# Kernel tuning notes

Measured on AMD Instinct MI355X. Metric: run time of the kernel, lower is better.

## Reference

```python
import jax, jax.numpy as jnp
import numpy as np

B, N, D, H = 4, 4096, 1024, 16
HD = D // H  # 64
EPS_NORM = 1e-12  # F.normalize eps
EPS_LN = 1e-5     # layernorm eps


def setup_inputs() -> dict:
    key = jax.random.key(0)
    ks = jax.random.split(key, 9)
    s = 0.02
    return {
        "x": jax.random.normal(ks[0], (B, N, D), jnp.float32),
        "Wq": jax.random.normal(ks[1], (D, D), jnp.float32) * s,
        "Wk": jax.random.normal(ks[2], (D, D), jnp.float32) * s,
        "Wv": jax.random.normal(ks[3], (D, D), jnp.float32) * s,
        "Wf": jax.random.normal(ks[4], (H, D), jnp.float32) * s,
        "Wg1": jax.random.normal(ks[5], (HD, D), jnp.float32) * s,
        "Wg2": jax.random.normal(ks[6], (D, HD), jnp.float32) * s,
        "ln_w": jnp.ones((D,), jnp.float32),
        "Wo": jax.random.normal(ks[7], (D, D), jnp.float32) * s,
    }


def _silu(x):
    return x * jax.nn.sigmoid(x)


def _simple_gla(q, k, v, f):
    # q,k,v: [B,N,H,HD], f: [B,N,H] log-decay. Recurrence:
    #   S_t = exp(f_t) * S_{t-1} + k_t v_t^T ;  o_t = q_t^T S_t  (scale=1)
    qT = jnp.moveaxis(q, 1, 0)  # [N,B,H,HD]
    kT = jnp.moveaxis(k, 1, 0)
    vT = jnp.moveaxis(v, 1, 0)
    fT = jnp.moveaxis(f, 1, 0)  # [N,B,H]

    def step(S, inp):
        qt, kt, vt, ft = inp
        S = jnp.exp(ft)[..., None, None] * S + kt[..., :, None] * vt[..., None, :]
        o = jnp.einsum('bhk,bhkv->bhv', qt, S)
        return S, o

    S0 = jnp.zeros((q.shape[0], q.shape[2], q.shape[3], v.shape[3]), q.dtype)
    _, o = jax.lax.scan(step, S0, (qT, kT, vT, fT))
    return jnp.moveaxis(o, 0, 1)  # [B,N,H,HD]


def reference(x, Wq, Wk, Wv, Wf, Wg1, Wg2, ln_w, Wo):
    b, n, d = x.shape
    q = _silu(x @ Wq.T).reshape(b, n, H, HD)
    k = _silu(x @ Wk.T).reshape(b, n, H, HD)
    v = _silu(x @ Wv.T).reshape(b, n, H, HD)
    f = jax.nn.log_sigmoid(x @ Wf.T)  # [B,N,H] scalar per-head log decay
    # F.normalize(k, p=2, dim=-1)
    k = k / jnp.maximum(jnp.linalg.norm(k, axis=-1, keepdims=True), EPS_NORM)

    o = _simple_gla(q, k, v, f).reshape(b, n, d)

    # output gate: sigmoid(Linear(d->hd) -> Linear(hd->d))
    gate = jax.nn.sigmoid((x @ Wg1.T) @ Wg2.T)
    o = o * gate

    # layernorm without bias
    mu = jnp.mean(o, axis=-1, keepdims=True)
    xc = o - mu
    var = jnp.mean(xc * xc, axis=-1, keepdims=True)
    o = xc / jnp.sqrt(var + EPS_LN) * ln_w

    return o @ Wo.T
```

## Files before the change

kernel.cpp:

```cpp
#include <hip/hip_runtime.h>
#include <stdint.h>


#define NWIDE 3200

typedef __attribute__((ext_vector_type(4))) float f32x4;
typedef __attribute__((ext_vector_type(4))) unsigned short u16x4;
typedef __attribute__((ext_vector_type(8))) unsigned short u16x8;
typedef __attribute__((ext_vector_type(8))) __bf16 bf16x8;

__device__ __forceinline__ float bf2f(unsigned short u) {
    union { unsigned int i; float f; } c; c.i = ((unsigned int)u) << 16; return c.f;
}
__device__ __forceinline__ unsigned short f2bf(float f) {
    union { float f; unsigned int i; } c; c.f = f;
    return (unsigned short)((c.i + 0x7fffu + ((c.i >> 16) & 1u)) >> 16);
}
__device__ __forceinline__ float siluf(float x) { return x / (1.f + __expf(-x)); }
__device__ __forceinline__ float logsigf(float z) {
    return (z >= 0.f) ? -log1pf(__expf(-z)) : (z - log1pf(__expf(z)));
}
__device__ __forceinline__ f32x4 MFMA(bf16x8 a, bf16x8 b, f32x4 c) {
    return __builtin_amdgcn_mfma_f32_16x16x32_bf16(a, b, c, 0, 0, 0);
}
__device__ __forceinline__ void lds16(const void* g, void* l) {
    __builtin_amdgcn_global_load_lds(
        (const __attribute__((address_space(1))) unsigned int*)(uintptr_t)g,
        (__attribute__((address_space(3))) unsigned int*)(unsigned int)(uintptr_t)l,
        16, 0, 0);
}

__global__ __launch_bounds__(256) void k_convert(const float* __restrict__ src,
                                                 unsigned short* __restrict__ dst, int n4) {
    int i = blockIdx.x * 256 + threadIdx.x;
    if (i >= n4) return;
    f32x4 v = ((const f32x4*)src)[i];
    u16x4 o;
#pragma unroll
    for (int e = 0; e < 4; e++) o[e] = f2bf(v[e]);
    ((u16x4*)dst)[i] = o;
}

__global__ __launch_bounds__(256) void k_wcat(const float* __restrict__ Wq, const float* __restrict__ Wk,
                                              const float* __restrict__ Wv, const float* __restrict__ Wf,
                                              const float* __restrict__ Wg1, unsigned short* __restrict__ Wcat) {
    const int r = blockIdx.x, t = threadIdx.x;
    const float* src = nullptr; int sr = r;
    if (r < 1024) { src = Wq; }
    else if (r < 2048) { src = Wk; sr = r - 1024; }
    else if (r < 3072) { src = Wv; sr = r - 2048; }
    else if (r < 3088) { src = Wf; sr = r - 3072; }
    else if (r < 3152) { src = Wg1; sr = r - 3088; }
    u16x4 o;
    if (src) {
        f32x4 v = *(const f32x4*)&src[(size_t)sr * 1024 + 4 * t];
#pragma unroll
        for (int e = 0; e < 4; e++) o[e] = f2bf(v[e]);
    } else {
        o[0] = 0; o[1] = 0; o[2] = 0; o[3] = 0;
    }
    *(u16x4*)&Wcat[(size_t)r * 1024 + 4 * t] = o;
}

template <int MODE>
__global__ __launch_bounds__(256)
void k_gemm(const unsigned short* __restrict__ A, const unsigned short* __restrict__ Bw,
            void* __restrict__ outp, float* __restrict__ zbuf, int M, int N, int K, int ldOut) {
    __shared__ __align__(16) unsigned short As[128 * 32];
    __shared__ __align__(16) unsigned short Bs[128 * 32];
    const int tid = threadIdx.x;
    const int w = tid >> 6, lane = tid & 63;
    const int m0 = blockIdx.x * 128, n0 = blockIdx.y * 128;
    const int srow = lane >> 2, scol = (lane & 3) * 8;
    const int fr = lane & 15, fg = lane >> 4;
    const int wr = w >> 1, wc = w & 1;
    f32x4 acc[4][4] = {};
    const int kc = K >> 5;
    for (int kt = 0; kt < kc; ++kt) {
        const int k0 = kt << 5;
        __syncthreads();
        {
            const unsigned short* ga = A + (size_t)(m0 + 32 * w + srow) * K + k0 + scol;
            lds16(ga, &As[(32 * w) * 32]);
            const unsigned short* ga2 = A + (size_t)(m0 + 32 * w + 16 + srow) * K + k0 + scol;
            lds16(ga2, &As[(32 * w + 16) * 32]);
            const unsigned short* gb = Bw + (size_t)(n0 + 32 * w + srow) * K + k0 + scol;
            lds16(gb, &Bs[(32 * w) * 32]);
            const unsigned short* gb2 = Bw + (size_t)(n0 + 32 * w + 16 + srow) * K + k0 + scol;
            lds16(gb2, &Bs[(32 * w + 16) * 32]);
        }
        __syncthreads();
        bf16x8 av[4], bv[4];
#pragma unroll
        for (int i = 0; i < 4; i++) av[i] = *(const bf16x8*)&As[(64 * wr + 16 * i + fr) * 32 + fg * 8];
#pragma unroll
        for (int j = 0; j < 4; j++) bv[j] = *(const bf16x8*)&Bs[(64 * wc + 16 * j + fr) * 32 + fg * 8];
#pragma unroll
        for (int i = 0; i < 4; i++)
#pragma unroll
            for (int j = 0; j < 4; j++)
                acc[i][j] = MFMA(av[i], bv[j], acc[i][j]);
    }
    const int nb = n0 + 64 * wc;
    if (MODE == 1) {
        float* O = (float*)outp;
#pragma unroll
        for (int i = 0; i < 4; i++)
#pragma unroll
            for (int j = 0; j < 4; j++) {
                const int gc = nb + 16 * j + fr;
#pragma unroll
                for (int r = 0; r < 4; r++)
                    O[(size_t)(m0 + 64 * wr + 16 * i + 4 * fg + r) * ldOut + gc] = acc[i][j][r];
            }
        return;
    }
    unsigned short* Y = (unsigned short*)outp;
    if (nb >= 3072) {
#pragma unroll
        for (int i = 0; i < 4; i++)
#pragma unroll
            for (int j = 0; j < 4; j++) {
                const int gc = nb + 16 * j + fr;
#pragma unroll
                for (int r = 0; r < 4; r++) {
                    const int gr = m0 + 64 * wr + 16 * i + 4 * fg + r;
                    const float v = acc[i][j][r];
                    if (gc < 3088) {
                        if (gc >= 3072) zbuf[gr * 16 + (gc - 3072)] = v;
                    } else if (gc < 3152) {
                        Y[(size_t)gr * ldOut + gc] = f2bf(v);
                    }
                }
            }
    } else {
#pragma unroll
        for (int i = 0; i < 4; i++)
#pragma unroll
            for (int j = 0; j < 4; j++) {
                const int gc = nb + 16 * j + fr;
#pragma unroll
                for (int r = 0; r < 4; r++)
                    Y[(size_t)(m0 + 64 * wr + 16 * i + 4 * fg + r) * ldOut + gc] = f2bf(acc[i][j][r]);
            }
    }
}

__global__ void k_cumsum(const float* __restrict__ zbuf, float* __restrict__ cbuf) {
    const int cid = blockIdx.x, t = threadIdx.x;
    const int bh = cid >> 6, ic = cid & 63;
    const int b = bh >> 4, h = bh & 15;
    float v = logsigf(zbuf[(size_t)(b * 4096 + ic * 64 + t) * 16 + h]);
#pragma unroll
    for (int off = 1; off < 64; off <<= 1) {
        float u = __shfl_up(v, (unsigned)off, 64);
        if (t >= off) v += u;
    }
    cbuf[(size_t)cid * 64 + t] = v;
}

__global__ __launch_bounds__(256)
void k_chunk_kv(const unsigned short* __restrict__ Y, const float* __restrict__ cbuf,
                unsigned short* __restrict__ St) {
    __shared__ __align__(16) unsigned short Kt[64 * 72];
    __shared__ __align__(16) unsigned short Vt[64 * 72];
    __shared__ float cs[64];
    const int cid = blockIdx.x, tid = threadIdx.x;
    const int bh = cid >> 6, ic = cid & 63;
    const int b = bh >> 4, h = bh & 15;
    if (tid < 64) cs[tid] = cbuf[(size_t)cid * 64 + tid];
    __syncthreads();
    const int s = tid >> 2, c0 = (tid & 3) << 4;
    const float wdec = __expf(cs[63] - cs[s]);
    const size_t rowg = (size_t)(b * 4096 + ic * 64 + s) * NWIDE;
    u16x8 k0v = *(const u16x8*)&Y[rowg + 1024 + h * 64 + c0];
    u16x8 k1v = *(const u16x8*)&Y[rowg + 1024 + h * 64 + c0 + 8];
    u16x8 v0v = *(const u16x8*)&Y[rowg + 2048 + h * 64 + c0];
    u16x8 v1v = *(const u16x8*)&Y[rowg + 2048 + h * 64 + c0 + 8];
    float kf[16]; float ss = 0.f;
#pragma unroll
    for (int e = 0; e < 8; e++) { kf[e] = siluf(bf2f(k0v[e])); ss += kf[e] * kf[e]; }
#pragma unroll
    for (int e = 0; e < 8; e++) { kf[8 + e] = siluf(bf2f(k1v[e])); ss += kf[8 + e] * kf[8 + e]; }
    ss += __shfl_xor(ss, 1, 64);
    ss += __shfl_xor(ss, 2, 64);
    const float sc = wdec / fmaxf(sqrtf(ss), 1e-12f);
#pragma unroll
    for (int e = 0; e < 8; e++) {
        Kt[(c0 + e) * 72 + s] = f2bf(kf[e] * sc);
        Kt[(c0 + 8 + e) * 72 + s] = f2bf(kf[8 + e] * sc);
        Vt[(c0 + e) * 72 + s] = f2bf(siluf(bf2f(v0v[e])));
        Vt[(c0 + 8 + e) * 72 + s] = f2bf(siluf(bf2f(v1v[e])));
    }
    __syncthreads();
    const int w = tid >> 6, lane = tid & 63;
    const int fr = lane & 15, fg = lane >> 4;
    f32x4 acc[4] = {};
#pragma unroll
    for (int ks = 0; ks < 2; ks++) {
        bf16x8 a = *(const bf16x8*)&Kt[(16 * w + fr) * 72 + ks * 32 + fg * 8];
#pragma unroll
        for (int j = 0; j < 4; j++)
            acc[j] = MFMA(a, *(const bf16x8*)&Vt[(16 * j + fr) * 72 + ks * 32 + fg * 8], acc[j]);
    }
    unsigned short* outp = St + (size_t)cid * 4096;
#pragma unroll
    for (int j = 0; j < 4; j++)
#pragma unroll
        for (int r = 0; r < 4; r++)
            outp[(16 * w + 4 * fg + r) * 64 + 16 * j + fr] = f2bf(acc[j][r]);
}

__global__ void k_scan(unsigned short* __restrict__ St, const float* __restrict__ cbuf) {
    const int bh = blockIdx.x >> 4;
    const int e = ((blockIdx.x & 15) << 8) + threadIdx.x;
    float S = 0.f;
    const size_t base = (size_t)bh * 64 * 4096 + e;
    for (int i = 0; i < 64; i++) {
        const float d = __expf(cbuf[(bh * 64 + i) * 64 + 63]);
        const float m = bf2f(St[base + (size_t)i * 4096]);
        St[base + (size_t)i * 4096] = f2bf(S);
        S = d * S + m;
    }
}

__global__ __launch_bounds__(256)
void k_chunk_out(const unsigned short* __restrict__ Y, const float* __restrict__ cbuf,
                 const unsigned short* __restrict__ St, const unsigned short* __restrict__ Wg2b,
                 unsigned short* __restrict__ og) {
    __shared__ __align__(16) unsigned short Qs[64 * 72];
    __shared__ __align__(16) unsigned short Ks[64 * 72];
    __shared__ __align__(16) unsigned short Vt[64 * 72];
    __shared__ __align__(16) unsigned short S0[64 * 72];
    __shared__ __align__(16) unsigned short G1[64 * 72];
    __shared__ __align__(16) unsigned short W2[64 * 72];
    __shared__ __align__(16) unsigned short Pl[4 * 16 * 72];
    __shared__ float cs[64];
    const int cid = blockIdx.x, tid = threadIdx.x;
    const int bh = cid >> 6, ic = cid & 63;
    const int b = bh >> 4, h = bh & 15;
    if (tid < 64) cs[tid] = cbuf[(size_t)cid * 64 + tid];
    const int s = tid >> 2, c0 = (tid & 3) << 4;
    const size_t rowg = (size_t)(b * 4096 + ic * 64 + s) * NWIDE;
    {
        u16x8 q0 = *(const u16x8*)&Y[rowg + h * 64 + c0];
        u16x8 q1 = *(const u16x8*)&Y[rowg + h * 64 + c0 + 8];
        u16x8 o0, o1;
#pragma unroll
        for (int e = 0; e < 8; e++) { o0[e] = f2bf(siluf(bf2f(q0[e]))); o1[e] = f2bf(siluf(bf2f(q1[e]))); }
        *(u16x8*)&Qs[s * 72 + c0] = o0;
        *(u16x8*)&Qs[s * 72 + c0 + 8] = o1;
    }
    {
        u16x8 k0v = *(const u16x8*)&Y[rowg + 1024 + h * 64 + c0];
        u16x8 k1v = *(const u16x8*)&Y[rowg + 1024 + h * 64 + c0 + 8];
        float kf[16]; float ssn = 0.f;
#pragma unroll
        for (int e = 0; e < 8; e++) { kf[e] = siluf(bf2f(k0v[e])); ssn += kf[e] * kf[e]; }
#pragma unroll
        for (int e = 0; e < 8; e++) { kf[8 + e] = siluf(bf2f(k1v[e])); ssn += kf[8 + e] * kf[8 + e]; }
        ssn += __shfl_xor(ssn, 1, 64);
        ssn += __shfl_xor(ssn, 2, 64);
        const float scn = 1.f / fmaxf(sqrtf(ssn), 1e-12f);
        u16x8 o0, o1;
#pragma unroll
        for (int e = 0; e < 8; e++) { o0[e] = f2bf(kf[e] * scn); o1[e] = f2bf(kf[8 + e] * scn); }
        *(u16x8*)&Ks[s * 72 + c0] = o0;
        *(u16x8*)&Ks[s * 72 + c0 + 8] = o1;
    }
    *(u16x8*)&G1[s * 72 + c0] = *(const u16x8*)&Y[rowg + 3088 + c0];
    *(u16x8*)&G1[s * 72 + c0 + 8] = *(const u16x8*)&Y[rowg + 3088 + c0 + 8];
    *(u16x8*)&W2[s * 72 + c0] = *(const u16x8*)&Wg2b[(size_t)(h * 64 + s) * 64 + c0];
    *(u16x8*)&W2[s * 72 + c0 + 8] = *(const u16x8*)&Wg2b[(size_t)(h * 64 + s) * 64 + c0 + 8];
    {
        u16x8 v0v = *(const u16x8*)&Y[rowg + 2048 + h * 64 + c0];
        u16x8 v1v = *(const u16x8*)&Y[rowg + 2048 + h * 64 + c0 + 8];
        u16x8 s0v = *(const u16x8*)&St[(size_t)cid * 4096 + s * 64 + c0];
        u16x8 s1v = *(const u16x8*)&St[(size_t)cid * 4096 + s * 64 + c0 + 8];
#pragma unroll
        for (int e = 0; e < 8; e++) {
            Vt[(c0 + e) * 72 + s] = f2bf(siluf(bf2f(v0v[e])));
            Vt[(c0 + 8 + e) * 72 + s] = f2bf(siluf(bf2f(v1v[e])));
            S0[(c0 + e) * 72 + s] = s0v[e];
            S0[(c0 + 8 + e) * 72 + s] = s1v[e];
        }
    }
    __syncthreads();
    const int w = tid >> 6, lane = tid & 63;
    const int fr = lane & 15, fg = lane >> 4;
    bf16x8 aq[2];
#pragma unroll
    for (int ks = 0; ks < 2; ks++) aq[ks] = *(const bf16x8*)&Qs[(16 * w + fr) * 72 + ks * 32 + fg * 8];
    f32x4 sc[4] = {};
#pragma unroll
    for (int ks = 0; ks < 2; ks++)
#pragma unroll
        for (int j = 0; j < 4; j++)
            sc[j] = MFMA(aq[ks], *(const bf16x8*)&Ks[(16 * j + fr) * 72 + ks * 32 + fg * 8], sc[j]);
    const int tl = 16 * w + 4 * fg;
#pragma unroll
    for (int j = 0; j < 4; j++)
#pragma unroll
        for (int r = 0; r < 4; r++) {
            const int tt = tl + r, ss2 = 16 * j + fr;
            float p = (ss2 <= tt) ? sc[j][r] * __expf(cs[tt] - cs[ss2]) : 0.f;
            Pl[w * (16 * 72) + (4 * fg + r) * 72 + ss2] = f2bf(p);
        }
    __syncthreads();
    f32x4 ov[4] = {};
#pragma unroll
    for (int ks = 0; ks < 2; ks++) {
        bf16x8 ap = *(const bf16x8*)&Pl[w * (16 * 72) + fr * 72 + ks * 32 + fg * 8];
#pragma unroll
        for (int j = 0; j < 4; j++)
            ov[j] = MFMA(ap, *(const bf16x8*)&Vt[(16 * j + fr) * 72 + ks * 32 + fg * 8], ov[j]);
    }
    f32x4 qs[4] = {};
#pragma unroll
    for (int ks = 0; ks < 2; ks++)
#pragma unroll
        for (int j = 0; j < 4; j++)
            qs[j] = MFMA(aq[ks], *(const bf16x8*)&S0[(16 * j + fr) * 72 + ks * 32 + fg * 8], qs[j]);
    bf16x8 ag[2];
#pragma unroll
    for (int ks = 0; ks < 2; ks++) ag[ks] = *(const bf16x8*)&G1[(16 * w + fr) * 72 + ks * 32 + fg * 8];
    f32x4 gl[4] = {};
#pragma unroll
    for (int ks = 0; ks < 2; ks++)
#pragma unroll
        for (int j = 0; j < 4; j++)
            gl[j] = MFMA(ag[ks], *(const bf16x8*)&W2[(16 * j + fr) * 72 + ks * 32 + fg * 8], gl[j]);
#pragma unroll
    for (int j = 0; j < 4; j++)
#pragma unroll
        for (int r = 0; r < 4; r++) {
            const int tt = tl + r;
            const float o = ov[j][r] + __expf(cs[tt]) * qs[j][r];
            const float g = 1.f / (1.f + __expf(-gl[j][r]));
            og[(size_t)(b * 4096 + ic * 64 + tt) * 1024 + h * 64 + 16 * j + fr] = f2bf(o * g);
        }
}

__global__ __launch_bounds__(256)
void k_ln(unsigned short* __restrict__ og, const float* __restrict__ lnw) {
    __shared__ float red[8];
    const int r = blockIdx.x, t = threadIdx.x;
    unsigned short* p = og + (size_t)r * 1024;
    u16x4 a = *(u16x4*)&p[4 * t];
    float x[4]; float s = 0.f, ssum = 0.f;
#pragma unroll
    for (int e = 0; e < 4; e++) { x[e] = bf2f(a[e]); s += x[e]; ssum += x[e] * x[e]; }
#pragma unroll
    for (int m = 1; m < 64; m <<= 1) { s += __shfl_xor(s, m, 64); ssum += __shfl_xor(ssum, m, 64); }
    const int w = t >> 6;
    if ((t & 63) == 0) { red[w] = s; red[4 + w] = ssum; }
    __syncthreads();
    s = red[0] + red[1] + red[2] + red[3];
    ssum = red[4] + red[5] + red[6] + red[7];
    const float mu = s * (1.f / 1024.f);
    const float var = ssum * (1.f / 1024.f) - mu * mu;
    const float rs = rsqrtf(var + 1e-5f);
    u16x4 o;
#pragma unroll
    for (int e = 0; e < 4; e++) o[e] = f2bf((x[e] - mu) * rs * lnw[4 * t + e]);
    *(u16x4*)&p[4 * t] = o;
}

extern "C" void kernel_launch(void* const* d_in, const int* in_sizes, int n_in,
                              void* d_out, int out_size, void* d_ws, size_t ws_size,
                              hipStream_t stream) {
    const float* x = (const float*)d_in[0];
    const float* Wq = (const float*)d_in[1];
    const float* Wk = (const float*)d_in[2];
    const float* Wv = (const float*)d_in[3];
    const float* Wf = (const float*)d_in[4];
    const float* Wg1 = (const float*)d_in[5];
    const float* Wg2 = (const float*)d_in[6];
    const float* lnw = (const float*)d_in[7];
    const float* Wo = (const float*)d_in[8];
    char* ws = (char*)d_ws;
    unsigned short* xb = (unsigned short*)(ws + 0);
    unsigned short* Yb = (unsigned short*)(ws + 33554432LL);
    unsigned short* Wcat = (unsigned short*)(ws + 138412032LL);
    unsigned short* Wob = (unsigned short*)(ws + 144965632LL);
    unsigned short* Wg2b = (unsigned short*)(ws + 147062784LL);
    float* zbuf = (float*)(ws + 147193856LL);
    float* cbuf = (float*)(ws + 148242432LL);
    unsigned short* St = (unsigned short*)(ws + 149291008LL);
    unsigned short* og = xb;

    k_convert<<<16384, 256, 0, stream>>>(x, xb, 4194304);
    k_wcat<<<3200, 256, 0, stream>>>(Wq, Wk, Wv, Wf, Wg1, Wcat);
    k_convert<<<1024, 256, 0, stream>>>(Wo, Wob, 262144);
    k_convert<<<64, 256, 0, stream>>>(Wg2, Wg2b, 16384);
    k_gemm<0><<<dim3(128, 25), 256, 0, stream>>>(xb, Wcat, Yb, zbuf, 16384, 3200, 1024, 3200);
    k_cumsum<<<4096, 64, 0, stream>>>(zbuf, cbuf);
    k_chunk_kv<<<4096, 256, 0, stream>>>(Yb, cbuf, St);
    k_scan<<<1024, 256, 0, stream>>>(St, cbuf);
    k_chunk_out<<<4096, 256, 0, stream>>>(Yb, cbuf, St, Wg2b, og);
    k_ln<<<16384, 256, 0, stream>>>(og, lnw);
    k_gemm<1><<<dim3(128, 8), 256, 0, stream>>>(og, Wob, d_out, nullptr, 16384, 1024, 1024, 1024);
}
```

Baseline: 348.4 us.

## Double GEMM K-tile to 64 and XOR-swizzle LDS layout

The GEMM k-loop now stages 64-wide K slices instead of 32, which halves the number of barrier pairs per tile and doubles the MFMAs issued between syncs. LDS rows are stored with an XOR swizzle on 16-byte chunks, so the fragment reads avoid bank conflicts. LDS usage doubles to 32 KB per block, which may lower occupancy, and more fragment registers are live at once.

```diff
diff --git a/kernel.cpp b/kernel.cpp
--- a/kernel.cpp
+++ b/kernel.cpp
@@ -66,40 +66,49 @@
 __global__ __launch_bounds__(256)
 void k_gemm(const unsigned short* __restrict__ A, const unsigned short* __restrict__ Bw,
             void* __restrict__ outp, float* __restrict__ zbuf, int M, int N, int K, int ldOut) {
-    __shared__ __align__(16) unsigned short As[128 * 32];
-    __shared__ __align__(16) unsigned short Bs[128 * 32];
+    __shared__ __align__(16) unsigned short As[128 * 64];
+    __shared__ __align__(16) unsigned short Bs[128 * 64];
     const int tid = threadIdx.x;
     const int w = tid >> 6, lane = tid & 63;
     const int m0 = blockIdx.x * 128, n0 = blockIdx.y * 128;
-    const int srow = lane >> 2, scol = (lane & 3) * 8;
     const int fr = lane & 15, fg = lane >> 4;
     const int wr = w >> 1, wc = w & 1;
+    const int srow = lane >> 3;
+    const int schunk = (lane & 7) ^ (srow & 7);
     f32x4 acc[4][4] = {};
-    const int kc = K >> 5;
+    const int kc = K >> 6;
     for (int kt = 0; kt < kc; ++kt) {
-        const int k0 = kt << 5;
+        const int k0 = kt << 6;
         __syncthreads();
-        {
-            const unsigned short* ga = A + (size_t)(m0 + 32 * w + srow) * K + k0 + scol;
-            lds16(ga, &As[(32 * w) * 32]);
-            const unsigned short* ga2 = A + (size_t)(m0 + 32 * w + 16 + srow) * K + k0 + scol;
-            lds16(ga2, &As[(32 * w + 16) * 32]);
-            const unsigned short* gb = Bw + (size_t)(n0 + 32 * w + srow) * K + k0 + scol;
-            lds16(gb, &Bs[(32 * w) * 32]);
-            const unsigned short* gb2 = Bw + (size_t)(n0 + 32 * w + 16 + srow) * K + k0 + scol;
-            lds16(gb2, &Bs[(32 * w + 16) * 32]);
+#pragma unroll
+        for (int q = 0; q < 4; q++) {
+            const int rr = 32 * w + 8 * q;
+            lds16(A + (size_t)(m0 + rr + srow) * K + k0 + schunk * 8, &As[rr * 64]);
+            lds16(Bw + (size_t)(n0 + rr + srow) * K + k0 + schunk * 8, &Bs[rr * 64]);
         }
         __syncthreads();
-        bf16x8 av[4], bv[4];
-#pragma unroll
-        for (int i = 0; i < 4; i++) av[i] = *(const bf16x8*)&As[(64 * wr + 16 * i + fr) * 32 + fg * 8];
-#pragma unroll
-        for (int j = 0; j < 4; j++) bv[j] = *(const bf16x8*)&Bs[(64 * wc + 16 * j + fr) * 32 + fg * 8];
+        bf16x8 av[4][2], bv[4][2];
 #pragma unroll
         for (int i = 0; i < 4; i++)
 #pragma unroll
+            for (int ks = 0; ks < 2; ks++) {
+                const int row = 64 * wr + 16 * i + fr;
+                av[i][ks] = *(const bf16x8*)&As[row * 64 + (((ks * 4 + fg) ^ (row & 7)) << 3)];
+            }
+#pragma unroll
+        for (int j = 0; j < 4; j++)
+#pragma unroll
+            for (int ks = 0; ks < 2; ks++) {
+                const int row = 64 * wc + 16 * j + fr;
+                bv[j][ks] = *(const bf16x8*)&Bs[row * 64 + (((ks * 4 + fg) ^ (row & 7)) << 3)];
+            }
+#pragma unroll
+        for (int i = 0; i < 4; i++)
+#pragma unroll
             for (int j = 0; j < 4; j++)
-                acc[i][j] = MFMA(av[i], bv[j], acc[i][j]);
+#pragma unroll
+                for (int ks = 0; ks < 2; ks++)
+                    acc[i][j] = MFMA(av[i][ks], bv[j][ks], acc[i][j]);
     }
     const int nb = n0 + 64 * wc;
     if (MODE == 1) {
```

Result: faster. 340.1 us (-2.4%).
